# Performance work log

Measured on AMD Instinct MI355X. Metric: run time of the kernel, lower is better.

The kernel has to match this reference:

```python
import jax, jax.numpy as jnp
import numpy as np

B, D, N = 256, 256, 100000
NUM_CLUSTERS, NUM_CLASSES = 100, 1000


def setup_inputs() -> dict:
    key = jax.random.key(0)
    k1, k2, k3, k4, k5, k6 = jax.random.split(key, 6)
    return {
        "feature": jax.random.normal(k1, (B, D), dtype=jnp.float32),
        "feature_bank": jax.random.normal(k2, (N, D), dtype=jnp.float32),
        "cluster_label_bank": jax.random.randint(k3, (N,), 0, NUM_CLUSTERS, dtype=jnp.int64)
            if jax.config.jax_enable_x64 else jax.random.randint(k3, (N,), 0, NUM_CLUSTERS).astype(jnp.int32),
        "class_label_bank": jax.random.randint(k4, (N,), 0, NUM_CLASSES).astype(jnp.int32),
        "cluster_idx": jax.random.randint(k5, (B,), 0, NUM_CLUSTERS).astype(jnp.int32),
        "gt_label": jax.random.randint(k6, (B,), 0, NUM_CLASSES).astype(jnp.int32),
    }


def reference(feature, feature_bank, cluster_label_bank, class_label_bank, cluster_idx, gt_label):
    # Masks: primary = same cluster AND different class; fallback = different class only.
    cluster_label_bank = cluster_label_bank.astype(jnp.int32)
    same_cluster = cluster_label_bank[None, :] == cluster_idx[:, None].astype(jnp.int32)  # [B, N]
    diff_class = class_label_bank[None, :] != gt_label[:, None]                            # [B, N]
    mask_primary = same_cluster & diff_class
    has_primary = mask_primary.any(axis=1, keepdims=True)
    mask = jnp.where(has_primary, mask_primary, diff_class)  # [B, N]

    # Euclidean distances (torch.cdist p=2): ||a-b|| via expanded squared form.
    a2 = jnp.sum(feature * feature, axis=1)[:, None]              # [B, 1]
    b2 = jnp.sum(feature_bank * feature_bank, axis=1)[None, :]    # [1, N]
    d2 = a2 + b2 - 2.0 * (feature @ feature_bank.T)               # [B, N]
    dist = jnp.sqrt(jnp.maximum(d2, 0.0))

    # Masked argmin over the bank, then gather negatives.
    dist_masked = jnp.where(mask, dist, jnp.inf)
    neg_idx = jnp.argmin(dist_masked, axis=1)                     # [B]
    negatives = feature_bank[neg_idx]                             # [B, D]
    return negatives
```

## Files before the change

kernel.cpp:

```cpp
#include <hip/hip_runtime.h>
#include <climits>

typedef __attribute__((ext_vector_type(8))) short s8;
typedef __attribute__((ext_vector_type(4))) float f32x4;

#define BQ    256
#define DDIM  256
#define NBANK 100000
#define BN    64
#define NJB   ((NBANK + BN - 1) / BN)
#define SENT  1e30f

__device__ inline void splitElem(float x, s8& h, s8& l, int i) {
    unsigned u  = __float_as_uint(x);
    unsigned uh = (u + 0x8000u) & 0xFFFF0000u;
    h[i] = (short)(uh >> 16);
    float lf = x - __uint_as_float(uh);
    l[i] = (short)((__float_as_uint(lf) + 0x8000u) >> 16);
}

__device__ inline void split8(const float4 v0, const float4 v1, s8& h, s8& l) {
    splitElem(v0.x, h, l, 0); splitElem(v0.y, h, l, 1);
    splitElem(v0.z, h, l, 2); splitElem(v0.w, h, l, 3);
    splitElem(v1.x, h, l, 4); splitElem(v1.y, h, l, 5);
    splitElem(v1.z, h, l, 6); splitElem(v1.w, h, l, 7);
}

__device__ inline float sq8(const float4 v0, const float4 v1, float s) {
    s = fmaf(v0.x, v0.x, s); s = fmaf(v0.y, v0.y, s);
    s = fmaf(v0.z, v0.z, s); s = fmaf(v0.w, v0.w, s);
    s = fmaf(v1.x, v1.x, s); s = fmaf(v1.y, v1.y, s);
    s = fmaf(v1.z, v1.z, s); s = fmaf(v1.w, v1.w, s);
    return s;
}

__global__ __launch_bounds__(512) void split_feature(
    const float* __restrict__ feature, s8* __restrict__ fH, s8* __restrict__ fL)
{
    const int t    = blockIdx.x * 512 + threadIdx.x;
    const int lane = t & 63, ks = (t >> 6) & 7, rt = t >> 9;
    const int row  = rt * 16 + (lane & 15);
    const int k0   = ks * 32 + (lane >> 4) * 8;
    const float* p = feature + (size_t)row * DDIM + k0;
    const float4 v0 = *(const float4*)p;
    const float4 v1 = *(const float4*)(p + 4);
    s8 h, l;
    split8(v0, v1, h, l);
    fH[t] = h; fL[t] = l;
}

__global__ __launch_bounds__(1024, 8) void gemm_argmin_w16(
    const s8* __restrict__ fH, const s8* __restrict__ fL,
    const float* __restrict__ bank,
    const int* __restrict__ cluster_label, const int* __restrict__ class_label,
    const int* __restrict__ cluster_idx,  const int* __restrict__ gt_label,
    float* __restrict__ wsPV, int* __restrict__ wsPI,
    float* __restrict__ wsDV, int* __restrict__ wsDI)
{
    __shared__ __align__(16) s8 bHs[4 * 4 * 64];
    __shared__ __align__(16) s8 bLs[4 * 4 * 64];
    __shared__ float b2s[BN];
    __shared__ int clsS[BN], cluS[BN], rowGt[BQ], rowClu[BQ];

    const int tid = threadIdx.x;
    const int jb  = blockIdx.x;
    const int j0  = jb * BN;

    const int col = tid >> 4, q = tid & 15;
    const int ct_s = col >> 4, cl_s = col & 15;
    const int sl_s = q >> 2, o_s = q & 3;
    const int w = tid >> 6, lane = tid & 63;
    const int g = lane >> 4, c = lane & 15;

    int jcol = j0 + col; if (jcol >= NBANK) jcol = NBANK - 1;
    const float* gb = bank + (size_t)jcol * DDIM + q * 8;

    if (tid < BQ) {
        rowGt[tid]  = gt_label[tid];
        rowClu[tid] = cluster_idx[tid];
    }
    if (tid < BN) {
        int jg = j0 + tid; int jc = jg < NBANK ? jg : NBANK - 1;
        clsS[tid] = class_label[jc];
        cluS[tid] = cluster_label[jc];
    }
    float4 a0 = *(const float4*)(gb);
    float4 a1 = *(const float4*)(gb + 4);

    float sqa = 0.f;
    {
        s8 h, l;
        split8(a0, a1, h, l);
        sqa = sq8(a0, a1, sqa);
        const int wi = (((sl_s * 4 + ct_s) * 64 + o_s * 16 + cl_s)) ^ q;
        bHs[wi] = h; bLs[wi] = l;
    }
    __syncthreads();

    a0 = *(const float4*)(gb + 128);
    a1 = *(const float4*)(gb + 132);

    f32x4 acc[4];
    #pragma unroll
    for (int ct = 0; ct < 4; ++ct)
        acc[ct] = (f32x4){0.f, 0.f, 0.f, 0.f};

    #pragma unroll
    for (int sl = 0; sl < 4; ++sl) {
        const s8 aH = fH[(w * 8 + sl) * 64 + lane];
        const s8 aL = fL[(w * 8 + sl) * 64 + lane];
        const int rx = sl * 4 + g;
        #pragma unroll
        for (int ct = 0; ct < 4; ++ct) {
            const s8 bh = bHs[((sl * 4 + ct) * 64 + lane) ^ rx];
            const s8 bl = bLs[((sl * 4 + ct) * 64 + lane) ^ rx];
            acc[ct] = __builtin_amdgcn_mfma_f32_16x16x32_bf16(aH, bh, acc[ct], 0, 0, 0);
            acc[ct] = __builtin_amdgcn_mfma_f32_16x16x32_bf16(aH, bl, acc[ct], 0, 0, 0);
            acc[ct] = __builtin_amdgcn_mfma_f32_16x16x32_bf16(aL, bh, acc[ct], 0, 0, 0);
            acc[ct] = __builtin_amdgcn_mfma_f32_16x16x32_bf16(aL, bl, acc[ct], 0, 0, 0);
        }
    }
    __syncthreads();

    {
        s8 h, l;
        split8(a0, a1, h, l);
        sqa = sq8(a0, a1, sqa);
        const int wi = (((sl_s * 4 + ct_s) * 64 + o_s * 16 + cl_s)) ^ q;
        bHs[wi] = h; bLs[wi] = l;
    }
    sqa += __shfl_xor(sqa, 1);
    sqa += __shfl_xor(sqa, 2);
    sqa += __shfl_xor(sqa, 4);
    sqa += __shfl_xor(sqa, 8);
    if (q == 0) b2s[col] = sqa;
    __syncthreads();

    #pragma unroll
    for (int sl = 0; sl < 4; ++sl) {
        const s8 aH = fH[(w * 8 + 4 + sl) * 64 + lane];
        const s8 aL = fL[(w * 8 + 4 + sl) * 64 + lane];
        const int rx = sl * 4 + g;
        #pragma unroll
        for (int ct = 0; ct < 4; ++ct) {
            const s8 bh = bHs[((sl * 4 + ct) * 64 + lane) ^ rx];
            const s8 bl = bLs[((sl * 4 + ct) * 64 + lane) ^ rx];
            acc[ct] = __builtin_amdgcn_mfma_f32_16x16x32_bf16(aH, bh, acc[ct], 0, 0, 0);
            acc[ct] = __builtin_amdgcn_mfma_f32_16x16x32_bf16(aH, bl, acc[ct], 0, 0, 0);
            acc[ct] = __builtin_amdgcn_mfma_f32_16x16x32_bf16(aL, bh, acc[ct], 0, 0, 0);
            acc[ct] = __builtin_amdgcn_mfma_f32_16x16x32_bf16(aL, bl, acc[ct], 0, 0, 0);
        }
    }

    #pragma unroll
    for (int r = 0; r < 4; ++r) {
        const int row  = w * 16 + g * 4 + r;
        const int myGt = rowGt[row], myClu = rowClu[row];
        float bpv = SENT, bdv = SENT;
        int   bpi = INT_MAX, bdi = INT_MAX;
        #pragma unroll
        for (int ct = 0; ct < 4; ++ct) {
            const int jg = j0 + ct * 16 + c;
            const float sc = b2s[ct * 16 + c] - 2.f * acc[ct][r];
            if (jg < NBANK && clsS[ct * 16 + c] != myGt) {
                if (sc < bdv) { bdv = sc; bdi = jg; }
                if (cluS[ct * 16 + c] == myClu && sc < bpv) { bpv = sc; bpi = jg; }
            }
        }
        #pragma unroll
        for (int off = 1; off < 16; off <<= 1) {
            float vv = __shfl_xor(bpv, off); int ii = __shfl_xor(bpi, off);
            if (vv < bpv || (vv == bpv && ii < bpi)) { bpv = vv; bpi = ii; }
            vv = __shfl_xor(bdv, off); ii = __shfl_xor(bdi, off);
            if (vv < bdv || (vv == bdv && ii < bdi)) { bdv = vv; bdi = ii; }
        }
        if (c == 0) {
            const size_t o = (size_t)jb * BQ + row;
            wsPV[o] = bpv; wsPI[o] = bpi;
            wsDV[o] = bdv; wsDI[o] = bdi;
        }
    }
}

__global__ __launch_bounds__(256) void reduce_gather(
    const float* __restrict__ wsPV, const int* __restrict__ wsPI,
    const float* __restrict__ wsDV, const int* __restrict__ wsDI,
    const float* __restrict__ bank, float* __restrict__ out)
{
    const int row = blockIdx.x, tid = threadIdx.x;
    float bpv = SENT, bdv = SENT;
    int   bpi = INT_MAX, bdi = INT_MAX;
    for (int b = tid; b < NJB; b += 256) {
        const size_t o = (size_t)b * BQ + row;
        float v = wsPV[o]; int ix = wsPI[o];
        if (v < bpv || (v == bpv && ix < bpi)) { bpv = v; bpi = ix; }
        v = wsDV[o]; ix = wsDI[o];
        if (v < bdv || (v == bdv && ix < bdi)) { bdv = v; bdi = ix; }
    }
    #pragma unroll
    for (int off = 32; off > 0; off >>= 1) {
        float v = __shfl_down(bpv, off); int ix = __shfl_down(bpi, off);
        if (v < bpv || (v == bpv && ix < bpi)) { bpv = v; bpi = ix; }
        v = __shfl_down(bdv, off); ix = __shfl_down(bdi, off);
        if (v < bdv || (v == bdv && ix < bdi)) { bdv = v; bdi = ix; }
    }
    __shared__ float swPV[4], swDV[4];
    __shared__ int   swPI[4], swDI[4];
    __shared__ int   sIdx;
    const int lane = tid & 63, wv = tid >> 6;
    if (lane == 0) { swPV[wv] = bpv; swPI[wv] = bpi; swDV[wv] = bdv; swDI[wv] = bdi; }
    __syncthreads();
    if (tid == 0) {
        float pv = swPV[0]; int pi = swPI[0];
        float dv = swDV[0]; int di = swDI[0];
        #pragma unroll
        for (int w = 1; w < 4; ++w) {
            if (swPV[w] < pv || (swPV[w] == pv && swPI[w] < pi)) { pv = swPV[w]; pi = swPI[w]; }
            if (swDV[w] < dv || (swDV[w] == dv && swDI[w] < di)) { dv = swDV[w]; di = swDI[w]; }
        }
        sIdx = (pi != INT_MAX) ? pi : ((di != INT_MAX) ? di : 0);
    }
    __syncthreads();
    out[row * DDIM + tid] = bank[(size_t)sIdx * DDIM + tid];
}

extern "C" void kernel_launch(void* const* d_in, const int* in_sizes, int n_in,
                              void* d_out, int out_size, void* d_ws, size_t ws_size,
                              hipStream_t stream) {
    const float* feature       = (const float*)d_in[0];
    const float* bank          = (const float*)d_in[1];
    const int*   cluster_label = (const int*)d_in[2];
    const int*   class_label   = (const int*)d_in[3];
    const int*   cluster_idx   = (const int*)d_in[4];
    const int*   gt_label      = (const int*)d_in[5];
    float* out = (float*)d_out;

    s8* fH = (s8*)d_ws;
    s8* fL = fH + 8192;
    float* base = (float*)((char*)d_ws + 2 * 8192 * sizeof(s8));
    const size_t per = (size_t)BQ * NJB;
    float* wsPV = base;
    int*   wsPI = (int*)base + per;
    float* wsDV = base + 2 * per;
    int*   wsDI = (int*)base + 3 * per;

    hipLaunchKernelGGL(split_feature, dim3(16), dim3(512), 0, stream, feature, fH, fL);
    hipLaunchKernelGGL(gemm_argmin_w16, dim3(NJB), dim3(1024), 0, stream,
                       fH, fL, bank, cluster_label, class_label, cluster_idx, gt_label,
                       wsPV, wsPI, wsDV, wsDI);
    hipLaunchKernelGGL(reduce_gather, dim3(BQ), dim3(256), 0, stream,
                       wsPV, wsPI, wsDV, wsDI, bank, out);
}
```

Baseline: 256.1 us.

## Split query rows across two 512-thread blocks per bank tile

The fused GEMM-argmin kernel now launches two 512-thread blocks per 64-column bank tile, each handling half of the 256 query rows, instead of one 1024-thread block. Each thread loads and splits 16 bank floats instead of 8, and the LDS swizzle and row-sum reduction are adjusted to match. The aim is finer-grained blocks that schedule more flexibly. The cost is that every bank tile is read from memory and split into bf16 hi/lo twice, doubling that conversion work and the bank traffic unless it hits in cache.

```diff
diff --git a/kernel.cpp b/kernel.cpp
--- a/kernel.cpp
+++ b/kernel.cpp
@@ -49,7 +49,7 @@
     fH[t] = h; fL[t] = l;
 }
 
-__global__ __launch_bounds__(1024, 8) void gemm_argmin_w16(
+__global__ __launch_bounds__(512, 4) void gemm_argmin_msplit(
     const s8* __restrict__ fH, const s8* __restrict__ fL,
     const float* __restrict__ bank,
     const int* __restrict__ cluster_label, const int* __restrict__ class_label,
@@ -60,24 +60,26 @@
     __shared__ __align__(16) s8 bHs[4 * 4 * 64];
     __shared__ __align__(16) s8 bLs[4 * 4 * 64];
     __shared__ float b2s[BN];
-    __shared__ int clsS[BN], cluS[BN], rowGt[BQ], rowClu[BQ];
+    __shared__ int clsS[BN], cluS[BN], rowGt[128], rowClu[128];
 
     const int tid = threadIdx.x;
-    const int jb  = blockIdx.x;
+    const int bb  = blockIdx.x;
+    const int jb  = bb >> 1, mh = bb & 1;
     const int j0  = jb * BN;
-
-    const int col = tid >> 4, q = tid & 15;
+    const int r0  = mh * 128;
+
+    const int col = tid >> 3, q = tid & 7;
     const int ct_s = col >> 4, cl_s = col & 15;
-    const int sl_s = q >> 2, o_s = q & 3;
+    const int sl_s = q >> 1, p_s = q & 1;
     const int w = tid >> 6, lane = tid & 63;
     const int g = lane >> 4, c = lane & 15;
 
     int jcol = j0 + col; if (jcol >= NBANK) jcol = NBANK - 1;
-    const float* gb = bank + (size_t)jcol * DDIM + q * 8;
-
-    if (tid < BQ) {
-        rowGt[tid]  = gt_label[tid];
-        rowClu[tid] = cluster_idx[tid];
+    const float* gb = bank + (size_t)jcol * DDIM + q * 16;
+
+    if (tid < 128) {
+        rowGt[tid]  = gt_label[r0 + tid];
+        rowClu[tid] = cluster_idx[r0 + tid];
     }
     if (tid < BN) {
         int jg = j0 + tid; int jc = jg < NBANK ? jg : NBANK - 1;
@@ -86,30 +88,40 @@
     }
     float4 a0 = *(const float4*)(gb);
     float4 a1 = *(const float4*)(gb + 4);
+    float4 a2 = *(const float4*)(gb + 8);
+    float4 a3 = *(const float4*)(gb + 12);
 
     float sqa = 0.f;
     {
         s8 h, l;
         split8(a0, a1, h, l);
         sqa = sq8(a0, a1, sqa);
-        const int wi = (((sl_s * 4 + ct_s) * 64 + o_s * 16 + cl_s)) ^ q;
+        int wi = (((sl_s * 4 + ct_s) * 64 + (p_s * 2 + 0) * 16 + cl_s)) ^ q;
+        bHs[wi] = h; bLs[wi] = l;
+        split8(a2, a3, h, l);
+        sqa = sq8(a2, a3, sqa);
+        wi = (((sl_s * 4 + ct_s) * 64 + (p_s * 2 + 1) * 16 + cl_s)) ^ q;
         bHs[wi] = h; bLs[wi] = l;
     }
     __syncthreads();
 
     a0 = *(const float4*)(gb + 128);
     a1 = *(const float4*)(gb + 132);
+    a2 = *(const float4*)(gb + 136);
+    a3 = *(const float4*)(gb + 140);
 
     f32x4 acc[4];
     #pragma unroll
     for (int ct = 0; ct < 4; ++ct)
         acc[ct] = (f32x4){0.f, 0.f, 0.f, 0.f};
 
+    const int RT = mh * 8 + w;
+
     #pragma unroll
     for (int sl = 0; sl < 4; ++sl) {
-        const s8 aH = fH[(w * 8 + sl) * 64 + lane];
-        const s8 aL = fL[(w * 8 + sl) * 64 + lane];
-        const int rx = sl * 4 + g;
+        const s8 aH = fH[(RT * 8 + sl) * 64 + lane];
+        const s8 aL = fL[(RT * 8 + sl) * 64 + lane];
+        const int rx = sl * 2 + (lane >> 5);
         #pragma unroll
         for (int ct = 0; ct < 4; ++ct) {
             const s8 bh = bHs[((sl * 4 + ct) * 64 + lane) ^ rx];
@@ -126,21 +138,24 @@
         s8 h, l;
         split8(a0, a1, h, l);
         sqa = sq8(a0, a1, sqa);
-        const int wi = (((sl_s * 4 + ct_s) * 64 + o_s * 16 + cl_s)) ^ q;
+        int wi = (((sl_s * 4 + ct_s) * 64 + (p_s * 2 + 0) * 16 + cl_s)) ^ q;
+        bHs[wi] = h; bLs[wi] = l;
+        split8(a2, a3, h, l);
+        sqa = sq8(a2, a3, sqa);
+        wi = (((sl_s * 4 + ct_s) * 64 + (p_s * 2 + 1) * 16 + cl_s)) ^ q;
         bHs[wi] = h; bLs[wi] = l;
     }
     sqa += __shfl_xor(sqa, 1);
     sqa += __shfl_xor(sqa, 2);
     sqa += __shfl_xor(sqa, 4);
-    sqa += __shfl_xor(sqa, 8);
     if (q == 0) b2s[col] = sqa;
     __syncthreads();
 
     #pragma unroll
     for (int sl = 0; sl < 4; ++sl) {
-        const s8 aH = fH[(w * 8 + 4 + sl) * 64 + lane];
-        const s8 aL = fL[(w * 8 + 4 + sl) * 64 + lane];
-        const int rx = sl * 4 + g;
+        const s8 aH = fH[(RT * 8 + 4 + sl) * 64 + lane];
+        const s8 aL = fL[(RT * 8 + 4 + sl) * 64 + lane];
+        const int rx = sl * 2 + (lane >> 5);
         #pragma unroll
         for (int ct = 0; ct < 4; ++ct) {
             const s8 bh = bHs[((sl * 4 + ct) * 64 + lane) ^ rx];
@@ -154,8 +169,8 @@
 
     #pragma unroll
     for (int r = 0; r < 4; ++r) {
-        const int row  = w * 16 + g * 4 + r;
-        const int myGt = rowGt[row], myClu = rowClu[row];
+        const int lrow = w * 16 + g * 4 + r;
+        const int myGt = rowGt[lrow], myClu = rowClu[lrow];
         float bpv = SENT, bdv = SENT;
         int   bpi = INT_MAX, bdi = INT_MAX;
         #pragma unroll
@@ -175,7 +190,7 @@
             if (vv < bdv || (vv == bdv && ii < bdi)) { bdv = vv; bdi = ii; }
         }
         if (c == 0) {
-            const size_t o = (size_t)jb * BQ + row;
+            const size_t o = (size_t)jb * BQ + r0 + lrow;
             wsPV[o] = bpv; wsPI[o] = bpi;
             wsDV[o] = bdv; wsDI[o] = bdi;
         }
@@ -245,7 +260,7 @@
     int*   wsDI = (int*)base + 3 * per;
 
     hipLaunchKernelGGL(split_feature, dim3(16), dim3(512), 0, stream, feature, fH, fL);
-    hipLaunchKernelGGL(gemm_argmin_w16, dim3(NJB), dim3(1024), 0, stream,
+    hipLaunchKernelGGL(gemm_argmin_msplit, dim3(NJB * 2), dim3(512), 0, stream,
                        fH, fL, bank, cluster_label, class_label, cluster_idx, gt_label,
                        wsPV, wsPI, wsDV, wsDI);
     hipLaunchKernelGGL(reduce_gather, dim3(BQ), dim3(256), 0, stream,
```

After: 230.1 us. 10.1% less time.
